# Performance work log

Measured on AMD Instinct MI355X. Metric: run time of the kernel, lower is better.

The kernel has to match this reference:

```python
import jax, jax.numpy as jnp
import numpy as np
import math

B, L, D = 8, 2048, 768
ORDER, EMB = 128, 5
FFT = 2 * L
MIN_DECAY = math.log(0.01) / 1.5   # slow_decay_pct = 1.5
MAX_DECAY = math.log(0.01) / 0.3   # fast_decay_pct = 0.3
SHIFT = 0.0


def _pos_emb(seq_len, emb_dim):
    # pos_emb_init from the source: [t, Re(z), Im(z)] with bands = (emb_dim-1)//2
    bands = (emb_dim - 1) // 2
    t = jnp.linspace(0.0, 1.0, seq_len)[None, :, None]
    t_res = jnp.linspace(0.0, seq_len - 1, seq_len)[None, :, None]
    w = 2.0 * jnp.pi * t_res / seq_len
    f = jnp.linspace(1e-4, bands - 1, bands)[None, None]
    zc = jnp.exp(-1j * f * w)
    return jnp.concatenate([t, zc.real, zc.imag], axis=-1).astype(jnp.float32)  # (1, L, EMB)


def setup_inputs() -> dict:
    key = jax.random.key(0)
    ks = jax.random.split(key, 16)
    s = 0.02
    return {
        "u": jax.random.normal(ks[0], (B, L, D), jnp.float32),
        "in_W": jax.random.normal(ks[1], (D, 3 * D), jnp.float32) * s,
        "in_b": jnp.zeros((3 * D,), jnp.float32),
        "out_W": jax.random.normal(ks[2], (D, D), jnp.float32) * s,
        "out_b": jnp.zeros((D,), jnp.float32),
        "x1_s": jax.random.normal(ks[3], (D, 4), jnp.float32) * 0.25,
        "x2_s": jax.random.normal(ks[4], (D, 4), jnp.float32) * 0.25,
        "v_s": jax.random.normal(ks[5], (D, 4), jnp.float32) * 0.25,
        "x1_sb": jax.random.normal(ks[6], (D,), jnp.float32) * 0.1,
        "x2_sb": jax.random.normal(ks[7], (D,), jnp.float32) * 0.1,
        "v_sb": jax.random.normal(ks[8], (D,), jnp.float32) * 0.1,
        "D_bias": jax.random.normal(ks[9], (D,), jnp.float32),
        "z": _pos_emb(L, EMB),
        "sin_freq": 10.0 * jnp.ones((1, ORDER), jnp.float32),   # hyena_w = 10
        "eo_mat": jax.random.normal(ks[10], (1, EMB, ORDER), jnp.float32) * 0.3,
        "eo_bias": jnp.zeros((1, ORDER), jnp.float32),
        "oo1_mat": jax.random.normal(ks[11], (1, ORDER, ORDER), jnp.float32) * 0.08,
        "oo1_bias": jnp.zeros((1, ORDER), jnp.float32),
        "oo2_mat": jax.random.normal(ks[12], (1, ORDER, ORDER), jnp.float32) * 0.08,
        "oo2_bias": jnp.zeros((1, ORDER), jnp.float32),
        "oh_mat": jax.random.normal(ks[13], (1, ORDER, D), jnp.float32) * 0.08,
    }


def _depthwise4(x, w, b):
    # torch Conv1d(groups=3D, kernel=4, padding=3) truncated to [:L] == causal conv, left pad 3
    out = jax.lax.conv_general_dilated(
        x, w[:, None, :], window_strides=(1,), padding=[(3, 0)],
        dimension_numbers=("NCH", "OIH", "NCH"), feature_group_count=x.shape[1])
    return out + b[None, :, None]


def _hyena_filter(z, sin_freq, eo_mat, eo_bias, oo1_mat, oo1_bias, oo2_mat, oo2_bias, oh_mat):
    # then exponential decay modulation (exp_mod_in_place_fwd), channels=1, reverse=0.
    f = sin_freq[:, None, :]                                       # (1, 1, ORDER)
    h = jnp.sin(f * (jnp.einsum("cle,ceo->clo", z, eo_mat) + eo_bias[:, None, :]))
    h = jnp.sin(f * (jnp.einsum("clo,cop->clp", h, oo1_mat) + oo1_bias[:, None, :]))
    h = jnp.sin(f * (jnp.einsum("clo,cop->clp", h, oo2_mat) + oo2_bias[:, None, :]))
    k = jnp.einsum("clo,coh->clh", h, oh_mat)                      # (1, L, D)
    t = jnp.linspace(0.0, 1.0, k.shape[1])
    deltas = jnp.abs(jnp.linspace(MIN_DECAY, MAX_DECAY, k.shape[2]))
    k = k * (jnp.exp(-t[None, :, None] * deltas[None, None, :]) + SHIFT)
    return k[0].T                                                  # (D, L)


def _forward(u, in_W, in_b, out_W, out_b, x1_s, x2_s, v_s, x1_sb, x2_sb, v_sb,
             D_bias, z, sin_freq, eo_mat, eo_bias, oo1_mat, oo1_bias,
             oo2_mat, oo2_bias, oh_mat):
    seqlen = u.shape[1]
    k = _hyena_filter(z, sin_freq, eo_mat, eo_bias, oo1_mat, oo1_bias, oo2_mat, oo2_bias, oh_mat)
    x1x2v = u @ in_W + in_b                                        # (B, L, 3D)
    x1, x2, v = jnp.split(x1x2v, 3, axis=-1)
    x1 = jnp.transpose(x1, (0, 2, 1))                              # (B, D, L)
    x2 = jnp.transpose(x2, (0, 2, 1))
    v = jnp.transpose(v, (0, 2, 1))
    x1 = _depthwise4(x1, x1_s, x1_sb)
    x2 = _depthwise4(x2, x2_s, x2_sb)
    v = _depthwise4(v, v_s, v_sb)
    v = v * x1                                                     # first gate
    k_f = jnp.fft.rfft(k.astype(jnp.float32), n=FFT)               # (D, FFT//2+1)
    v_f = jnp.fft.rfft(v.astype(jnp.float32), n=FFT)               # (B, D, FFT//2+1)
    y = jnp.fft.irfft(v_f * k_f[None], n=FFT)[..., :seqlen]        # long FFT conv
    y = y + v * D_bias[None, :, None]                              # skip term
    y = y * x2                                                     # second gate
    y = jnp.transpose(y, (0, 2, 1))                                # (B, L, D)
    return y @ out_W + out_b


def reference(u, in_W, in_b, out_W, out_b, x1_s, x2_s, v_s, x1_sb, x2_sb, v_sb,
              D_bias, z, sin_freq, eo_mat, eo_bias, oo1_mat, oo1_bias,
              oo2_mat, oo2_bias, oh_mat):
    return _forward(u, in_W, in_b, out_W, out_b, x1_s, x2_s, v_s, x1_sb, x2_sb, v_sb,
                    D_bias, z, sin_freq, eo_mat, eo_bias, oo1_mat, oo1_bias,
                    oo2_mat, oo2_bias, oh_mat)
```

## Files before the change

kernel.cpp:

```cpp
#include <hip/hip_runtime.h>


typedef __bf16 bf16x8 __attribute__((ext_vector_type(8)));
typedef float  f32x4  __attribute__((ext_vector_type(4)));

#define AS1 __attribute__((address_space(1)))
#define AS3 __attribute__((address_space(3)))
#define GLD16(gp, lp) __builtin_amdgcn_global_load_lds((AS1 void*)(void*)(gp), (AS3 void*)(void*)(lp), 16, 0, 0)

#define LGKM_BAR       __asm__ __volatile__("s_waitcnt lgkmcnt(0)\n\ts_barrier" ::: "memory")
#define VM_LGKM_BAR(N) __asm__ __volatile__("s_waitcnt vmcnt(" #N ") lgkmcnt(0)\n\ts_barrier" ::: "memory")

__device__ __forceinline__ unsigned short f2b(float f) {
    unsigned u = __builtin_bit_cast(unsigned, f);
    unsigned r = (u + 0x7fffu + ((u >> 16) & 1u)) >> 16;
    return (unsigned short)r;
}
__device__ __forceinline__ float b2f_lo(unsigned u) {
    return __builtin_bit_cast(float, u << 16);
}
__device__ __forceinline__ float b2f_hi(unsigned u) {
    return __builtin_bit_cast(float, u & 0xffff0000u);
}

__device__ __forceinline__ float2 cmul(float2 a, float2 b) {
    return make_float2(a.x * b.x - a.y * b.y, a.x * b.y + a.y * b.x);
}
__device__ __forceinline__ float2 cadd(float2 a, float2 b) { return make_float2(a.x + b.x, a.y + b.y); }
__device__ __forceinline__ float2 csub(float2 a, float2 b) { return make_float2(a.x - b.x, a.y - b.y); }

#define TWO_PI 6.283185307179586f

#define BFLY(i,j)   { float2 ta=x[i], tb=x[j]; x[i]=cadd(ta,tb); x[j]=csub(ta,tb); }
#define BFLYW(i,j,w){ float2 ta=x[i], tb=x[j]; x[i]=cadd(ta,tb); x[j]=cmul(csub(ta,tb),(w)); }
#define BFLYI(i,j)  { float2 ta=x[i], tb=x[j]; x[i]=cadd(ta,tb); float2 tt=csub(ta,tb); x[j]=make_float2(-dd*tt.y, dd*tt.x); }
#define CSWAP(i,j)  { float2 tt=x[i]; x[i]=x[j]; x[j]=tt; }

template<int DIR, bool UZ>
__device__ __forceinline__ void dft16(float2* x) {
    const float dd = (float)DIR;
    const float C1 = 0.92387953251128674f, S1 = 0.38268343236508977f, R2 = 0.70710678118654752f;
    const float2 W1 = make_float2( C1, dd*S1);
    const float2 W2 = make_float2( R2, dd*R2);
    const float2 W3 = make_float2( S1, dd*C1);
    const float2 W5 = make_float2(-S1, dd*C1);
    const float2 W6 = make_float2(-R2, dd*R2);
    const float2 W7 = make_float2(-C1, dd*S1);
    if (UZ) {
        x[8]  = x[0];
        x[9]  = cmul(x[1], W1);
        x[10] = cmul(x[2], W2);
        x[11] = cmul(x[3], W3);
        x[12] = make_float2(-dd*x[4].y, dd*x[4].x);
        x[13] = cmul(x[5], W5);
        x[14] = cmul(x[6], W6);
        x[15] = cmul(x[7], W7);
    } else {
        BFLY(0,8); BFLYW(1,9,W1); BFLYW(2,10,W2); BFLYW(3,11,W3);
        BFLYI(4,12); BFLYW(5,13,W5); BFLYW(6,14,W6); BFLYW(7,15,W7);
    }
    BFLY(0,4);  BFLYW(1,5,W2);  BFLYI(2,6);   BFLYW(3,7,W6);
    BFLY(8,12); BFLYW(9,13,W2); BFLYI(10,14); BFLYW(11,15,W6);
    BFLY(0,2);  BFLYI(1,3);  BFLY(4,6);   BFLYI(5,7);
    BFLY(8,10); BFLYI(9,11); BFLY(12,14); BFLYI(13,15);
    BFLY(0,1); BFLY(2,3); BFLY(4,5); BFLY(6,7);
    BFLY(8,9); BFLY(10,11); BFLY(12,13); BFLY(14,15);
    CSWAP(1,8); CSWAP(2,4); CSWAP(3,12); CSWAP(5,10); CSWAP(7,14); CSWAP(11,13);
}

__device__ __forceinline__ void twiddle16(float2* x, float ang) {
    float s, c; __sincosf(ang, &s, &c);
    const float2 u1  = make_float2(c, s);
    const float2 u2  = cmul(u1, u1);
    const float2 u3  = cmul(u2, u1);
    const float2 u4  = cmul(u2, u2);
    const float2 u8  = cmul(u4, u4);
    const float2 u12 = cmul(u8, u4);
    x[1]  = cmul(x[1],  u1);
    x[2]  = cmul(x[2],  u2);
    x[3]  = cmul(x[3],  u3);
    x[4]  = cmul(x[4],  u4);
    x[5]  = cmul(x[5],  cmul(u4, u1));
    x[6]  = cmul(x[6],  cmul(u4, u2));
    x[7]  = cmul(x[7],  cmul(u4, u3));
    x[8]  = cmul(x[8],  u8);
    x[9]  = cmul(x[9],  cmul(u8, u1));
    x[10] = cmul(x[10], cmul(u8, u2));
    x[11] = cmul(x[11], cmul(u8, u3));
    x[12] = cmul(x[12], u12);
    x[13] = cmul(x[13], cmul(u12, u1));
    x[14] = cmul(x[14], cmul(u12, u2));
    x[15] = cmul(x[15], cmul(u12, u3));
}

__device__ __forceinline__ int ph1(int row, int col) { return row * 256 + (col ^ row); }
__device__ __forceinline__ int ph2(int row, int col) { return row * 16 + (col ^ (row & 15)); }

__device__ __forceinline__ void fft4096_fwd(float2* x, float2* lds, int t) {
    dft16<-1, true>(x);
    twiddle16(x, -(float)t * (TWO_PI / 4096.0f));
    #pragma unroll
    for (int k1 = 0; k1 < 16; ++k1) lds[ph1(k1, t)] = x[k1];
    __syncthreads();
    const int hi = t >> 4, lo = t & 15;
    #pragma unroll
    for (int t1 = 0; t1 < 16; ++t1) x[t1] = lds[ph1(hi, t1 * 16 + lo)];
    dft16<-1, false>(x);
    twiddle16(x, -(float)lo * (TWO_PI / 256.0f));
    __syncthreads();
    #pragma unroll
    for (int k2 = 0; k2 < 16; ++k2) lds[ph2(t, k2)] = x[k2];
    __syncthreads();
    #pragma unroll
    for (int t0 = 0; t0 < 16; ++t0) x[t0] = lds[ph2(hi * 16 + t0, lo)];
    dft16<-1, false>(x);
}

__device__ __forceinline__ void fft4096_inv(float2* x, float2* lds, int t) {
    const int hi = t >> 4, lo = t & 15;
    dft16<1, false>(x);
    __syncthreads();
    #pragma unroll
    for (int t0 = 0; t0 < 16; ++t0) lds[ph2(hi * 16 + t0, lo)] = x[t0];
    __syncthreads();
    #pragma unroll
    for (int k2 = 0; k2 < 16; ++k2) x[k2] = lds[ph2(t, k2)];
    twiddle16(x, (float)lo * (TWO_PI / 256.0f));
    dft16<1, false>(x);
    __syncthreads();
    #pragma unroll
    for (int t1 = 0; t1 < 16; ++t1) lds[ph1(hi, t1 * 16 + lo)] = x[t1];
    __syncthreads();
    #pragma unroll
    for (int k1 = 0; k1 < 16; ++k1) x[k1] = lds[ph1(k1, t)];
    twiddle16(x, (float)t * (TWO_PI / 4096.0f));
    dft16<1, false>(x);
}

__global__ __launch_bounds__(256) void filter_k_kernel(
    const float* __restrict__ z, const float* __restrict__ sf,
    const float* __restrict__ eo, const float* __restrict__ eo_b,
    const float* __restrict__ oo1, const float* __restrict__ oo1_b,
    const float* __restrict__ oo2, const float* __restrict__ oo2_b,
    const float* __restrict__ oh, float* __restrict__ kfil)
{
    __shared__ float h3buf[4][128];
    __shared__ float htmp[2][128];
    const int t = threadIdx.x;
    const int l0 = blockIdx.x * 4;
    const int half = t >> 7;
    const int o = t & 127;
    const float sfo = sf[o];
    for (int p = 0; p < 2; ++p) {
        const int li = p * 2 + half;
        const int l = l0 + li;
        float a = eo_b[o];
        #pragma unroll
        for (int e = 0; e < 5; ++e) a += z[l * 5 + e] * eo[e * 128 + o];
        htmp[half][o] = sinf(sfo * a);
        __syncthreads();
        float a2 = oo1_b[o];
        for (int q = 0; q < 128; ++q) a2 += htmp[half][q] * oo1[q * 128 + o];
        const float h2 = sinf(sfo * a2);
        __syncthreads();
        htmp[half][o] = h2;
        __syncthreads();
        float a3 = oo2_b[o];
        for (int q = 0; q < 128; ++q) a3 += htmp[half][q] * oo2[q * 128 + o];
        h3buf[li][o] = sinf(sfo * a3);
        __syncthreads();
    }
    const float MIND = -3.070113457325394f;
    const float MAXD = -15.350567286626972f;
    for (int c = 0; c < 3; ++c) {
        const int h = t + c * 256;
        float acc[4];
        #pragma unroll
        for (int li = 0; li < 4; ++li) acc[li] = 0.f;
        for (int q = 0; q < 128; ++q) {
            const float w = oh[q * 768 + h];
            #pragma unroll
            for (int li = 0; li < 4; ++li) acc[li] += h3buf[li][q] * w;
        }
        const float delta = fabsf(MIND + (MAXD - MIND) * (float)h * (1.0f / 767.0f));
        #pragma unroll
        for (int li = 0; li < 4; ++li) {
            const int l = l0 + li;
            const float tt = (float)l * (1.0f / 2047.0f);
            kfil[h * 2048 + l] = acc[li] * expf(-tt * delta);
        }
    }
}

__global__ __launch_bounds__(256) void filter_fft_kernel(
    const float* __restrict__ kfil, const float* __restrict__ D_bias,
    float2* __restrict__ Kf)
{
    __shared__ __align__(16) float2 lds[4096];
    const int d = blockIdx.x, t = threadIdx.x;
    float2 x[16];
    #pragma unroll
    for (int r = 0; r < 8; ++r) x[r] = make_float2(kfil[d * 2048 + r * 256 + t], 0.f);
    fft4096_fwd(x, lds, t);
    const float db = D_bias[d];
    const float s = 1.0f / 4096.0f;
    #pragma unroll
    for (int k3 = 0; k3 < 16; ++k3)
        Kf[d * 4096 + k3 * 256 + t] = make_float2((x[k3].x + db) * s, x[k3].y * s);
}

__global__ __launch_bounds__(256) void convert_u_kernel(
    const float* __restrict__ u, unsigned short* __restrict__ ub)
{
    const int g = blockIdx.x * 256 + threadIdx.x;
    const float4 v = ((const float4*)u)[g];
    uint2 o;
    o.x = (unsigned)f2b(v.x) | ((unsigned)f2b(v.y) << 16);
    o.y = (unsigned)f2b(v.z) | ((unsigned)f2b(v.w) << 16);
    ((uint2*)ub)[g] = o;
}

__global__ __launch_bounds__(256) void transpose_W_kernel(
    const float* __restrict__ W, unsigned short* __restrict__ Wt, int K, int N)
{
    __shared__ float tile[32][33];
    const int n0 = blockIdx.x * 32, k0 = blockIdx.y * 32;
    const int tx = threadIdx.x & 31, ty = threadIdx.x >> 5;
    #pragma unroll
    for (int r = 0; r < 4; ++r) {
        const int kk = ty + r * 8;
        tile[kk][tx] = W[(k0 + kk) * N + n0 + tx];
    }
    __syncthreads();
    #pragma unroll
    for (int r = 0; r < 4; ++r) {
        const int nn = ty + r * 8;
        Wt[(n0 + nn) * K + k0 + tx] = f2b(tile[tx][nn]);
    }
}

__global__ __launch_bounds__(256) void transpose_Y_kernel(
    const unsigned short* __restrict__ Y, unsigned short* __restrict__ Yt)
{
    __shared__ unsigned short tile[32][34];
    const int bx = blockIdx.x;
    const int l0 = (bx & 63) * 32;
    const int tmp = bx >> 6;
    const int d0 = (tmp % 24) * 32;
    const int b  = tmp / 24;
    const int tx = threadIdx.x & 31, ty = threadIdx.x >> 5;
    #pragma unroll
    for (int r = 0; r < 4; ++r) {
        const int dd = ty + r * 8;
        tile[dd][tx] = Y[(b * 768 + d0 + dd) * 2048 + l0 + tx];
    }
    __syncthreads();
    #pragma unroll
    for (int r = 0; r < 4; ++r) {
        const int ll = ty + r * 8;
        Yt[(b * 2048 + l0 + ll) * 768 + d0 + tx] = tile[tx][ll];
    }
}

template<int TM, int TN, int WR, int WC, int MODE>
__global__ __launch_bounds__(512, 2) void gemm2ph_kernel(
    const unsigned short* __restrict__ A,
    const unsigned short* __restrict__ Bm,
    const float* __restrict__ bias,
    unsigned short* __restrict__ outb,
    float* __restrict__ outf)
{
    constexpr int MF = TM / WR / 16;
    constexpr int NF = TN / WC / 16;
    constexpr int QA = TM / 64;
    constexpr int QB = TN / 64;
    extern __shared__ __align__(16) unsigned short lds[];
    unsigned short* As = lds;
    unsigned short* Bs = lds + 2 * TM * 64;
    const int t = threadIdx.x;
    const int wv = t >> 6, lane = t & 63;
    const int row0 = (MODE == 0 ? blockIdx.y : blockIdx.x) * TM;
    const int col0 = (MODE == 0 ? blockIdx.x : blockIdx.y) * TN;
    const int wr = wv / WC, wc = wv % WC;
    const int frow = lane & 15, kc = lane >> 4;

    f32x4 acc[MF][NF] = {};

    const int srow = t >> 3;
    const int cdat = (t & 7) ^ (srow & 7);
    const unsigned short* gA = A  + (row0 + srow) * 768 + cdat * 8;
    const unsigned short* gB = Bm + (col0 + srow) * 768 + cdat * 8;

#define STAGE(buf, kt)                                                        \
    {                                                                         \
        _Pragma("unroll") for (int q = 0; q < QA; ++q)                        \
            GLD16(gA + q * 49152 + (kt) * 64,                                 \
                  (char*)As + (buf) * (TM * 128) + q * 8192 + wv * 1024);     \
        _Pragma("unroll") for (int q = 0; q < QB; ++q)                        \
            GLD16(gB + q * 49152 + (kt) * 64,                                 \
                  (char*)Bs + (buf) * (TN * 128) + q * 8192 + wv * 1024);     \
    }

#define HALF(buf, ks)                                                         \
    {                                                                         \
        bf16x8 aF[MF], bF[NF];                                                \
        _Pragma("unroll") for (int m = 0; m < MF; ++m) {                      \
            const int r = wr * (TM / WR) + m * 16 + frow;                     \
            aF[m] = *(const bf16x8*)(As + (buf) * (TM * 64) + r * 64 +        \
                                     ((((ks) * 4 + kc) ^ (r & 7)) << 3));     \
        }                                                                     \
        _Pragma("unroll") for (int n = 0; n < NF; ++n) {                      \
            const int r = wc * (TN / WC) + n * 16 + frow;                     \
            bF[n] = *(const bf16x8*)(Bs + (buf) * (TN * 64) + r * 64 +        \
                                     ((((ks) * 4 + kc) ^ (r & 7)) << 3));     \
        }                                                                     \
        __builtin_amdgcn_s_setprio(1);                                        \
        _Pragma("unroll") for (int m = 0; m < MF; ++m)                        \
        _Pragma("unroll") for (int n = 0; n < NF; ++n)                        \
            acc[m][n] = __builtin_amdgcn_mfma_f32_16x16x32_bf16(              \
                aF[m], bF[n], acc[m][n], 0, 0, 0);                            \
        __builtin_amdgcn_s_setprio(0);                                        \
    }

    STAGE(0, 0);
    STAGE(1, 1);
    VM_LGKM_BAR(7);

    HALF(0, 0); HALF(0, 1);
    VM_LGKM_BAR(0);

    #pragma unroll 1
    for (int kt = 1; kt <= 9; kt += 2) {
        STAGE(0, kt + 1);
        HALF(1, 0); HALF(1, 1);
        VM_LGKM_BAR(0);
        STAGE(1, kt + 2);
        HALF(0, 0); HALF(0, 1);
        VM_LGKM_BAR(0);
    }

    HALF(1, 0); HALF(1, 1);
#undef STAGE
#undef HALF

    if (MODE == 0) {
        const int part = row0 / 768;
        const int bb = col0 / 2048;
        unsigned short* Xp = outb + (size_t)(part * 8 + bb) * 768 * 2048;
        const int drow0 = row0 - part * 768 + wr * (TM / WR) + kc * 4;
        const int lcol0 = col0 - bb * 2048 + wc * (TN / WC) + frow;
        #pragma unroll
        for (int m = 0; m < MF; ++m) {
            #pragma unroll
            for (int rr = 0; rr < 4; ++rr) {
                const int dd = drow0 + m * 16 + rr;
                const float bn = bias[row0 + wr * (TM / WR) + kc * 4 + m * 16 + rr];
                #pragma unroll
                for (int n = 0; n < NF; ++n)
                    Xp[dd * 2048 + lcol0 + n * 16] = f2b(acc[m][n][rr] + bn);
            }
        }
    } else {
        #pragma unroll
        for (int m = 0; m < MF; ++m) {
            #pragma unroll
            for (int rr = 0; rr < 4; ++rr) {
                const int mm = row0 + wr * (TM / WR) + kc * 4 + m * 16 + rr;
                #pragma unroll
                for (int n = 0; n < NF; ++n) {
                    const int nn = col0 + wc * (TN / WC) + n * 16 + frow;
                    outf[(size_t)mm * 768 + nn] = acc[m][n][rr] + bias[nn];
                }
            }
        }
    }
}

__device__ __forceinline__ void conv6(const unsigned short* __restrict__ p,
                                      const float* w, float bias, int t, float* out8)
{
    const uint4 m = *(const uint4*)(p + 8 * t);
    uint2 q = make_uint2(0u, 0u);
    if (t) q = *(const uint2*)(p + 8 * t - 4);
    float s[12];
    s[0] = b2f_lo(q.x); s[1] = b2f_hi(q.x); s[2] = b2f_lo(q.y); s[3] = b2f_hi(q.y);
    s[4] = b2f_lo(m.x); s[5] = b2f_hi(m.x); s[6] = b2f_lo(m.y); s[7] = b2f_hi(m.y);
    s[8] = b2f_lo(m.z); s[9] = b2f_hi(m.z); s[10] = b2f_lo(m.w); s[11] = b2f_hi(m.w);
    #pragma unroll
    for (int i = 0; i < 8; ++i)
        out8[i] = bias + w[0] * s[i + 1] + w[1] * s[i + 2] + w[2] * s[i + 3] + w[3] * s[i + 4];
}

__global__ __launch_bounds__(256) void fft_conv_kernel(
    const unsigned short* __restrict__ X, const float2* __restrict__ Kf,
    const float* __restrict__ x1_s, const float* __restrict__ x2_s, const float* __restrict__ v_s,
    const float* __restrict__ x1_sb, const float* __restrict__ x2_sb, const float* __restrict__ v_sb,
    unsigned short* __restrict__ Y)
{
    __shared__ __align__(16) float2 lds[4096];
    unsigned* ldsu = (unsigned*)lds;
    const int d = blockIdx.x, jp = blockIdx.y, t = threadIdx.x;
    const int b0 = jp * 2, b1 = b0 + 1;

    const unsigned short* px1a = X + ((size_t)(0 * 8 + b0) * 768 + d) * 2048;
    const unsigned short* pva  = X + ((size_t)(2 * 8 + b0) * 768 + d) * 2048;
    const unsigned short* px1b = X + ((size_t)(0 * 8 + b1) * 768 + d) * 2048;
    const unsigned short* pvb  = X + ((size_t)(2 * 8 + b1) * 768 + d) * 2048;

    {
        float w1[4], wv[4];
        #pragma unroll
        for (int j = 0; j < 4; ++j) { w1[j] = x1_s[d * 4 + j]; wv[j] = v_s[d * 4 + j]; }
        const float bc1 = x1_sb[d], bcv = v_sb[d];
        float pa[8];
        {
            float va[8], g[8];
            conv6(pva,  wv, bcv, t, va);
            conv6(px1a, w1, bc1, t, g);
            #pragma unroll
            for (int i = 0; i < 8; ++i) pa[i] = va[i] * g[i];
        }
        {
            float vb[8], g[8];
            conv6(pvb,  wv, bcv, t, vb);
            conv6(px1b, w1, bc1, t, g);
            unsigned vh[8];
            #pragma unroll
            for (int i = 0; i < 8; ++i)
                vh[i] = (unsigned)f2b(pa[i]) | ((unsigned)f2b(vb[i] * g[i]) << 16);
            *(uint4*)(ldsu + 8 * t)     = make_uint4(vh[0], vh[1], vh[2], vh[3]);
            *(uint4*)(ldsu + 8 * t + 4) = make_uint4(vh[4], vh[5], vh[6], vh[7]);
        }
    }
    __syncthreads();

    float2 x[16];
    #pragma unroll
    for (int r = 0; r < 8; ++r) {
        const unsigned u = ldsu[r * 256 + t];
        x[r] = make_float2(b2f_lo(u), b2f_hi(u));
    }
    __syncthreads();

    fft4096_fwd(x, lds, t);

    {
        const float2* kf = Kf + (size_t)d * 4096;
        #pragma unroll
        for (int c4 = 0; c4 < 4; ++c4) {
            float2 kr[4];
            #pragma unroll
            for (int j = 0; j < 4; ++j) kr[j] = kf[(c4 * 4 + j) * 256 + t];
            #pragma unroll
            for (int j = 0; j < 4; ++j) x[c4 * 4 + j] = cmul(x[c4 * 4 + j], kr[j]);
            __asm__ __volatile__("" ::: "memory");
        }
    }

    fft4096_inv(x, lds, t);

    __syncthreads();
    {
        const unsigned short* px2a = X + ((size_t)(1 * 8 + b0) * 768 + d) * 2048;
        const unsigned short* px2b = X + ((size_t)(1 * 8 + b1) * 768 + d) * 2048;
        float w2[4];
        #pragma unroll
        for (int j = 0; j < 4; ++j) w2[j] = x2_s[d * 4 + j];
        const float bc2 = x2_sb[d];
        float ga[8], gb[8];
        conv6(px2a, w2, bc2, t, ga);
        conv6(px2b, w2, bc2, t, gb);
        unsigned c2[8];
        #pragma unroll
        for (int i = 0; i < 8; ++i)
            c2[i] = (unsigned)f2b(ga[i]) | ((unsigned)f2b(gb[i]) << 16);
        *(uint4*)(ldsu + 8 * t)     = make_uint4(c2[0], c2[1], c2[2], c2[3]);
        *(uint4*)(ldsu + 8 * t + 4) = make_uint4(c2[4], c2[5], c2[6], c2[7]);
    }
    __syncthreads();

    unsigned short* ya = Y + ((size_t)b0 * 768 + d) * 2048;
    unsigned short* yb = Y + ((size_t)b1 * 768 + d) * 2048;
    #pragma unroll
    for (int n1 = 0; n1 < 8; ++n1) {
        const int l = n1 * 256 + t;
        const unsigned u = ldsu[l];
        ya[l] = f2b(x[n1].x * b2f_lo(u));
        yb[l] = f2b(x[n1].y * b2f_hi(u));
    }
}

extern "C" void kernel_launch(void* const* d_in, const int* in_sizes, int n_in,
                              void* d_out, int out_size, void* d_ws, size_t ws_size,
                              hipStream_t stream)
{
    (void)in_sizes; (void)n_in; (void)out_size; (void)ws_size;
    const float* u      = (const float*)d_in[0];
    const float* in_W   = (const float*)d_in[1];
    const float* in_b   = (const float*)d_in[2];
    const float* out_W  = (const float*)d_in[3];
    const float* out_b  = (const float*)d_in[4];
    const float* x1_s   = (const float*)d_in[5];
    const float* x2_s   = (const float*)d_in[6];
    const float* v_s    = (const float*)d_in[7];
    const float* x1_sb  = (const float*)d_in[8];
    const float* x2_sb  = (const float*)d_in[9];
    const float* v_sb   = (const float*)d_in[10];
    const float* D_bias = (const float*)d_in[11];
    const float* z      = (const float*)d_in[12];
    const float* sf     = (const float*)d_in[13];
    const float* eo     = (const float*)d_in[14];
    const float* eo_b   = (const float*)d_in[15];
    const float* oo1    = (const float*)d_in[16];
    const float* oo1_b  = (const float*)d_in[17];
    const float* oo2    = (const float*)d_in[18];
    const float* oo2_b  = (const float*)d_in[19];
    const float* oh     = (const float*)d_in[20];
    float* out = (float*)d_out;

    char* ws = (char*)d_ws;
    unsigned short* Xbf  = (unsigned short*)(ws + 0);
    unsigned short* Ybf  = (unsigned short*)(ws + 75497472);
    unsigned short* ubYt = (unsigned short*)(ws + 100663296);
    unsigned short* Wt   = (unsigned short*)(ws + 125829120);
    unsigned short* W2t  = (unsigned short*)(ws + 129368064);
    float*          kfil = (float*)(ws + 130547712);
    float2*         Kf   = (float2*)(ws + 136839168);

    static int attr_set = 0;
    if (!attr_set) {
        (void)hipFuncSetAttribute(
            reinterpret_cast<const void*>(&gemm2ph_kernel<192, 256, 2, 4, 0>),
            hipFuncAttributeMaxDynamicSharedMemorySize, 114688);
        (void)hipFuncSetAttribute(
            reinterpret_cast<const void*>(&gemm2ph_kernel<256, 192, 4, 2, 1>),
            hipFuncAttributeMaxDynamicSharedMemorySize, 114688);
        attr_set = 1;
    }

    filter_k_kernel<<<512, 256, 0, stream>>>(z, sf, eo, eo_b, oo1, oo1_b, oo2, oo2_b, oh, kfil);
    filter_fft_kernel<<<768, 256, 0, stream>>>(kfil, D_bias, Kf);
    convert_u_kernel<<<12288, 256, 0, stream>>>(u, ubYt);
    transpose_W_kernel<<<dim3(72, 24), 256, 0, stream>>>(in_W, Wt, 768, 2304);
    transpose_W_kernel<<<dim3(24, 24), 256, 0, stream>>>(out_W, W2t, 768, 768);
    gemm2ph_kernel<192, 256, 2, 4, 0><<<dim3(64, 12), 512, 114688, stream>>>(
        Wt, ubYt, in_b, Xbf, nullptr);
    fft_conv_kernel<<<dim3(768, 4), 256, 0, stream>>>(Xbf, Kf, x1_s, x2_s, v_s, x1_sb, x2_sb, v_sb, Ybf);
    transpose_Y_kernel<<<12288, 256, 0, stream>>>(Ybf, ubYt);
    gemm2ph_kernel<256, 192, 4, 2, 1><<<dim3(64, 4), 512, 114688, stream>>>(
        ubYt, W2t, out_b, nullptr, out);
}
```

Before: 348.2 us.

## Restructure GEMM main loop into eight-phase interleaved load/MFMA schedule

Replaces the two-phase double-buffered GEMM loop with an eight-phase schedule. Each K tile is split into four quadrant MFMA groups, and the A and B global-to-LDS loads are spread between them with finer barriers. The aim is to overlap global loads, LDS reads and MFMA work more evenly, so matrix cores are not stalled at the coarse barriers. In exchange it adds more barriers, more complex waitcnt accounting and a higher risk of ordering bugs in the buffer reuse.

```diff
diff --git a/kernel.cpp b/kernel.cpp
--- a/kernel.cpp
+++ b/kernel.cpp
@@ -263,7 +263,7 @@
 }
 
 template<int TM, int TN, int WR, int WC, int MODE>
-__global__ __launch_bounds__(512, 2) void gemm2ph_kernel(
+__global__ __launch_bounds__(512, 2) void gemm8ph_kernel(
     const unsigned short* __restrict__ A,
     const unsigned short* __restrict__ Bm,
     const float* __restrict__ bias,
@@ -272,6 +272,8 @@
 {
     constexpr int MF = TM / WR / 16;
     constexpr int NF = TN / WC / 16;
+    constexpr int MH = MF / 2;
+    constexpr int NH = NF / 2;
     constexpr int QA = TM / 64;
     constexpr int QB = TN / 64;
     extern __shared__ __align__(16) unsigned short lds[];
@@ -291,57 +293,115 @@
     const unsigned short* gA = A  + (row0 + srow) * 768 + cdat * 8;
     const unsigned short* gB = Bm + (col0 + srow) * 768 + cdat * 8;
 
-#define STAGE(buf, kt)                                                        \
-    {                                                                         \
-        _Pragma("unroll") for (int q = 0; q < QA; ++q)                        \
-            GLD16(gA + q * 49152 + (kt) * 64,                                 \
-                  (char*)As + (buf) * (TM * 128) + q * 8192 + wv * 1024);     \
-        _Pragma("unroll") for (int q = 0; q < QB; ++q)                        \
-            GLD16(gB + q * 49152 + (kt) * 64,                                 \
-                  (char*)Bs + (buf) * (TN * 128) + q * 8192 + wv * 1024);     \
-    }
-
-#define HALF(buf, ks)                                                         \
-    {                                                                         \
-        bf16x8 aF[MF], bF[NF];                                                \
-        _Pragma("unroll") for (int m = 0; m < MF; ++m) {                      \
-            const int r = wr * (TM / WR) + m * 16 + frow;                     \
-            aF[m] = *(const bf16x8*)(As + (buf) * (TM * 64) + r * 64 +        \
-                                     ((((ks) * 4 + kc) ^ (r & 7)) << 3));     \
-        }                                                                     \
-        _Pragma("unroll") for (int n = 0; n < NF; ++n) {                      \
-            const int r = wc * (TN / WC) + n * 16 + frow;                     \
-            bF[n] = *(const bf16x8*)(Bs + (buf) * (TN * 64) + r * 64 +        \
-                                     ((((ks) * 4 + kc) ^ (r & 7)) << 3));     \
-        }                                                                     \
-        __builtin_amdgcn_s_setprio(1);                                        \
-        _Pragma("unroll") for (int m = 0; m < MF; ++m)                        \
-        _Pragma("unroll") for (int n = 0; n < NF; ++n)                        \
-            acc[m][n] = __builtin_amdgcn_mfma_f32_16x16x32_bf16(              \
-                aF[m], bF[n], acc[m][n], 0, 0, 0);                            \
-        __builtin_amdgcn_s_setprio(0);                                        \
-    }
-
-    STAGE(0, 0);
-    STAGE(1, 1);
-    VM_LGKM_BAR(7);
-
-    HALF(0, 0); HALF(0, 1);
-    VM_LGKM_BAR(0);
+#define STG_Aq(buf, q, kt) GLD16(gA + (q) * 49152 + (kt),                     \
+        (char*)As + (buf) * (TM * 128) + (q) * 8192 + wv * 1024)
+#define STG_Bq(buf, q, kt) GLD16(gB + (q) * 49152 + (kt),                     \
+        (char*)Bs + (buf) * (TN * 128) + (q) * 8192 + wv * 1024)
+#define STG_A1(buf, kt) { STG_Aq(buf, 0, kt); STG_Aq(buf, 1, kt); }
+#define STG_A2(buf, kt) { _Pragma("unroll") for (int q = 2; q < QA; ++q) STG_Aq(buf, q, kt); }
+#define STG_B1(buf, kt) { STG_Bq(buf, 0, kt); STG_Bq(buf, 1, kt); }
+#define STG_B2(buf, kt) { _Pragma("unroll") for (int q = 2; q < QB; ++q) STG_Bq(buf, q, kt); }
+#define FENCE_QB { if constexpr (QB == 4) { VM_LGKM_BAR(4); } else { VM_LGKM_BAR(3); } }
+
+    bf16x8 aF[MH][2], bN0[NH][2], bN1[NH][2];
+
+#define READ_A(buf, mh)                                                        \
+    _Pragma("unroll") for (int m = 0; m < MH; ++m) {                           \
+        const int r = wr * (TM / WR) + ((mh) * MH + m) * 16 + frow;            \
+        aF[m][0] = *(const bf16x8*)(As + (buf) * (TM * 64) + r * 64 +          \
+                                    (((0 + kc) ^ (r & 7)) << 3));              \
+        aF[m][1] = *(const bf16x8*)(As + (buf) * (TM * 64) + r * 64 +          \
+                                    (((4 + kc) ^ (r & 7)) << 3));              \
+    }
+#define READ_B(buf, nh, arr)                                                   \
+    _Pragma("unroll") for (int n = 0; n < NH; ++n) {                           \
+        const int r = wc * (TN / WC) + ((nh) * NH + n) * 16 + frow;            \
+        arr[n][0] = *(const bf16x8*)(Bs + (buf) * (TN * 64) + r * 64 +         \
+                                     (((0 + kc) ^ (r & 7)) << 3));             \
+        arr[n][1] = *(const bf16x8*)(Bs + (buf) * (TN * 64) + r * 64 +         \
+                                     (((4 + kc) ^ (r & 7)) << 3));             \
+    }
+#define MFMA_Q(mh, nh, arr)                                                    \
+    __builtin_amdgcn_s_setprio(1);                                             \
+    _Pragma("unroll") for (int m = 0; m < MH; ++m)                             \
+    _Pragma("unroll") for (int n = 0; n < NH; ++n)                             \
+    _Pragma("unroll") for (int ks = 0; ks < 2; ++ks)                           \
+        acc[(mh) * MH + m][(nh) * NH + n] =                                    \
+            __builtin_amdgcn_mfma_f32_16x16x32_bf16(                           \
+                aF[m][ks], arr[n][ks], acc[(mh) * MH + m][(nh) * NH + n],      \
+                0, 0, 0);                                                      \
+    __builtin_amdgcn_s_setprio(0);
+
+    STG_A1(0, 0); STG_A2(0, 0); STG_B1(0, 0); STG_B2(0, 0);
+    STG_B1(1, 64); STG_B2(1, 64);
+    FENCE_QB;
 
     #pragma unroll 1
-    for (int kt = 1; kt <= 9; kt += 2) {
-        STAGE(0, kt + 1);
-        HALF(1, 0); HALF(1, 1);
+    for (int i = 0; i < 5; ++i) {
+        const int k1 = (2 * i + 1) * 64, k2 = (2 * i + 2) * 64, k3 = (2 * i + 3) * 64;
+        READ_A(0, 0); READ_B(0, 0, bN0);
+        STG_A1(1, k1);
+        MFMA_Q(0, 0, bN0);
+        LGKM_BAR;
+        READ_B(0, 1, bN1);
+        STG_A2(1, k1);
+        MFMA_Q(0, 1, bN1);
+        LGKM_BAR;
+        READ_A(0, 1);
+        STG_B1(0, k2);
+        MFMA_Q(1, 1, bN1);
+        LGKM_BAR;
+        STG_B2(0, k2);
+        MFMA_Q(1, 0, bN0);
+        FENCE_QB;
+        READ_A(1, 0); READ_B(1, 0, bN0);
+        STG_A1(0, k2);
+        MFMA_Q(0, 0, bN0);
+        LGKM_BAR;
+        READ_B(1, 1, bN1);
+        STG_A2(0, k2);
+        MFMA_Q(0, 1, bN1);
+        LGKM_BAR;
+        READ_A(1, 1);
+        STG_B1(1, k3);
+        MFMA_Q(1, 1, bN1);
+        LGKM_BAR;
+        STG_B2(1, k3);
+        MFMA_Q(1, 0, bN0);
+        FENCE_QB;
+    }
+
+    {
+        READ_A(0, 0); READ_B(0, 0, bN0);
+        STG_A1(1, 704);
+        MFMA_Q(0, 0, bN0);
+        LGKM_BAR;
+        READ_B(0, 1, bN1);
+        STG_A2(1, 704);
+        MFMA_Q(0, 1, bN1);
+        LGKM_BAR;
+        READ_A(0, 1);
+        MFMA_Q(1, 1, bN1);
+        LGKM_BAR;
+        MFMA_Q(1, 0, bN0);
         VM_LGKM_BAR(0);
-        STAGE(1, kt + 2);
-        HALF(0, 0); HALF(0, 1);
-        VM_LGKM_BAR(0);
-    }
-
-    HALF(1, 0); HALF(1, 1);
-#undef STAGE
-#undef HALF
+        READ_A(1, 0); READ_B(1, 0, bN0); READ_B(1, 1, bN1);
+        MFMA_Q(0, 0, bN0);
+        MFMA_Q(0, 1, bN1);
+        READ_A(1, 1);
+        MFMA_Q(1, 1, bN1);
+        MFMA_Q(1, 0, bN0);
+    }
+#undef READ_A
+#undef READ_B
+#undef MFMA_Q
+#undef STG_Aq
+#undef STG_Bq
+#undef STG_A1
+#undef STG_A2
+#undef STG_B1
+#undef STG_B2
+#undef FENCE_QB
 
     if (MODE == 0) {
         const int part = row0 / 768;
@@ -530,10 +590,10 @@
     static int attr_set = 0;
     if (!attr_set) {
         (void)hipFuncSetAttribute(
-            reinterpret_cast<const void*>(&gemm2ph_kernel<192, 256, 2, 4, 0>),
+            reinterpret_cast<const void*>(&gemm8ph_kernel<192, 256, 2, 4, 0>),
             hipFuncAttributeMaxDynamicSharedMemorySize, 114688);
         (void)hipFuncSetAttribute(
-            reinterpret_cast<const void*>(&gemm2ph_kernel<256, 192, 4, 2, 1>),
+            reinterpret_cast<const void*>(&gemm8ph_kernel<256, 192, 4, 2, 1>),
             hipFuncAttributeMaxDynamicSharedMemorySize, 114688);
         attr_set = 1;
     }
@@ -543,10 +603,10 @@
     convert_u_kernel<<<12288, 256, 0, stream>>>(u, ubYt);
     transpose_W_kernel<<<dim3(72, 24), 256, 0, stream>>>(in_W, Wt, 768, 2304);
     transpose_W_kernel<<<dim3(24, 24), 256, 0, stream>>>(out_W, W2t, 768, 768);
-    gemm2ph_kernel<192, 256, 2, 4, 0><<<dim3(64, 12), 512, 114688, stream>>>(
+    gemm8ph_kernel<192, 256, 2, 4, 0><<<dim3(64, 12), 512, 114688, stream>>>(
         Wt, ubYt, in_b, Xbf, nullptr);
     fft_conv_kernel<<<dim3(768, 4), 256, 0, stream>>>(Xbf, Kf, x1_s, x2_s, v_s, x1_sb, x2_sb, v_sb, Ybf);
     transpose_Y_kernel<<<12288, 256, 0, stream>>>(Ybf, ubYt);
-    gemm2ph_kernel<256, 192, 4, 2, 1><<<dim3(64, 4), 512, 114688, stream>>>(
+    gemm8ph_kernel<256, 192, 4, 2, 1><<<dim3(64, 4), 512, 114688, stream>>>(
         ubYt, W2t, out_b, nullptr, out);
 }
```

Result: slower. 361.3 us (+3.8%).

## Load in-projection GEMM B operand directly into registers, bypassing LDS

Applied to the files above, without the earlier changes.

Replaces the MODE-0 in-projection GEMM with a dedicated kernel that stages only the weight (A) tile through LDS. The B operand (the u activations) is loaded from global memory straight into MFMA register fragments, double-buffered across k-steps. This cuts LDS capacity per block (49 KB instead of 112 KB) and removes the LDS round trip for B. In exchange it adds register pressure and makes more direct, less coalesced global loads, with waitcnt values tuned by hand.

```diff
diff --git a/kernel.cpp b/kernel.cpp
--- a/kernel.cpp
+++ b/kernel.cpp
@@ -262,12 +262,122 @@
     }
 }
 
-template<int TM, int TN, int WR, int WC, int MODE>
+__global__ __launch_bounds__(512, 2) void gemm_bd_kernel(
+    const unsigned short* __restrict__ A,
+    const unsigned short* __restrict__ Bm,
+    const float* __restrict__ bias,
+    unsigned short* __restrict__ outb)
+{
+    extern __shared__ __align__(16) unsigned short lds[];
+    unsigned short* As = lds;
+    const int t = threadIdx.x;
+    const int wv = t >> 6, lane = t & 63;
+    const int row0 = blockIdx.y * 192;
+    const int col0 = blockIdx.x * 256;
+    const int wr = wv >> 2, wc = wv & 3;
+    const int frow = lane & 15, kc = lane >> 4;
+
+    f32x4 acc[6][4] = {};
+
+    const int srow = t >> 3;
+    const int cdat = (t & 7) ^ (srow & 7);
+    const unsigned short* gA = A + (row0 + srow) * 768 + cdat * 8;
+
+#define STG_A(buf, kt)                                                        \
+    { _Pragma("unroll") for (int q = 0; q < 3; ++q)                           \
+        GLD16(gA + q * 49152 + (kt) * 64,                                     \
+              (char*)As + (buf) * 24576 + q * 8192 + wv * 1024); }
+
+    const unsigned short* pB = Bm + (size_t)(col0 + wc * 64 + frow) * 768 + kc * 8;
+    bf16x8 bR0[4][2], bR1[4][2];
+
+#define LOADB(BR, tt)                                                         \
+    { _Pragma("unroll") for (int n = 0; n < 4; ++n) {                         \
+        BR[n][0] = *(const bf16x8*)(pB + (size_t)n * 12288 + (tt) * 64);      \
+        BR[n][1] = *(const bf16x8*)(pB + (size_t)n * 12288 + (tt) * 64 + 32); \
+    } }
+
+#define COMPUTE_HALF(bufbit, BR, mh)                                          \
+    {                                                                         \
+        bf16x8 aF[3][2];                                                      \
+        _Pragma("unroll") for (int m = 0; m < 3; ++m) {                       \
+            const int r = wr * 96 + ((mh) * 3 + m) * 16 + frow;               \
+            aF[m][0] = *(const bf16x8*)(As + (bufbit) * 12288 + r * 64 +      \
+                                        (((0 + kc) ^ (r & 7)) << 3));         \
+            aF[m][1] = *(const bf16x8*)(As + (bufbit) * 12288 + r * 64 +      \
+                                        (((4 + kc) ^ (r & 7)) << 3));         \
+        }                                                                     \
+        __builtin_amdgcn_s_setprio(1);                                        \
+        _Pragma("unroll") for (int m = 0; m < 3; ++m)                         \
+        _Pragma("unroll") for (int n = 0; n < 4; ++n)                         \
+        _Pragma("unroll") for (int ks = 0; ks < 2; ++ks)                      \
+            acc[(mh) * 3 + m][n] = __builtin_amdgcn_mfma_f32_16x16x32_bf16(   \
+                aF[m][ks], BR[n][ks], acc[(mh) * 3 + m][n], 0, 0, 0);         \
+        __builtin_amdgcn_s_setprio(0);                                        \
+    }
+
+    STG_A(0, 0);
+    LOADB(bR0, 0);
+    STG_A(1, 1);
+    LOADB(bR1, 1);
+    VM_LGKM_BAR(11);
+
+    COMPUTE_HALF(0, bR0, 0); COMPUTE_HALF(0, bR0, 1);
+    LOADB(bR0, 2);
+    VM_LGKM_BAR(8);
+
+    #pragma unroll 1
+    for (int i = 0; i < 4; ++i) {
+        const int to = 2 * i + 1, te = 2 * i + 2;
+        STG_A(0, to + 1);
+        COMPUTE_HALF(1, bR1, 0); COMPUTE_HALF(1, bR1, 1);
+        LOADB(bR1, to + 2);
+        VM_LGKM_BAR(8);
+        STG_A(1, te + 1);
+        COMPUTE_HALF(0, bR0, 0); COMPUTE_HALF(0, bR0, 1);
+        LOADB(bR0, te + 2);
+        VM_LGKM_BAR(8);
+    }
+
+    STG_A(0, 10);
+    COMPUTE_HALF(1, bR1, 0); COMPUTE_HALF(1, bR1, 1);
+    LOADB(bR1, 11);
+    VM_LGKM_BAR(8);
+
+    STG_A(1, 11);
+    COMPUTE_HALF(0, bR0, 0); COMPUTE_HALF(0, bR0, 1);
+    VM_LGKM_BAR(0);
+
+    COMPUTE_HALF(1, bR1, 0); COMPUTE_HALF(1, bR1, 1);
+#undef STG_A
+#undef LOADB
+#undef COMPUTE_HALF
+
+    {
+        const int part = row0 / 768;
+        const int bb = col0 / 2048;
+        unsigned short* Xp = outb + (size_t)(part * 8 + bb) * 768 * 2048;
+        const int drow0 = row0 - part * 768 + wr * 96 + kc * 4;
+        const int lcol0 = col0 - bb * 2048 + wc * 64 + frow;
+        #pragma unroll
+        for (int m = 0; m < 6; ++m) {
+            #pragma unroll
+            for (int rr = 0; rr < 4; ++rr) {
+                const int dd = drow0 + m * 16 + rr;
+                const float bn = bias[row0 + wr * 96 + kc * 4 + m * 16 + rr];
+                #pragma unroll
+                for (int n = 0; n < 4; ++n)
+                    Xp[dd * 2048 + lcol0 + n * 16] = f2b(acc[m][n][rr] + bn);
+            }
+        }
+    }
+}
+
+template<int TM, int TN, int WR, int WC>
 __global__ __launch_bounds__(512, 2) void gemm2ph_kernel(
     const unsigned short* __restrict__ A,
     const unsigned short* __restrict__ Bm,
     const float* __restrict__ bias,
-    unsigned short* __restrict__ outb,
     float* __restrict__ outf)
 {
     constexpr int MF = TM / WR / 16;
@@ -279,8 +389,8 @@
     unsigned short* Bs = lds + 2 * TM * 64;
     const int t = threadIdx.x;
     const int wv = t >> 6, lane = t & 63;
-    const int row0 = (MODE == 0 ? blockIdx.y : blockIdx.x) * TM;
-    const int col0 = (MODE == 0 ? blockIdx.x : blockIdx.y) * TN;
+    const int row0 = blockIdx.x * TM;
+    const int col0 = blockIdx.y * TN;
     const int wr = wv / WC, wc = wv % WC;
     const int frow = lane & 15, kc = lane >> 4;
 
@@ -343,34 +453,15 @@
 #undef STAGE
 #undef HALF
 
-    if (MODE == 0) {
-        const int part = row0 / 768;
-        const int bb = col0 / 2048;
-        unsigned short* Xp = outb + (size_t)(part * 8 + bb) * 768 * 2048;
-        const int drow0 = row0 - part * 768 + wr * (TM / WR) + kc * 4;
-        const int lcol0 = col0 - bb * 2048 + wc * (TN / WC) + frow;
-        #pragma unroll
-        for (int m = 0; m < MF; ++m) {
+    #pragma unroll
+    for (int m = 0; m < MF; ++m) {
+        #pragma unroll
+        for (int rr = 0; rr < 4; ++rr) {
+            const int mm = row0 + wr * (TM / WR) + kc * 4 + m * 16 + rr;
             #pragma unroll
-            for (int rr = 0; rr < 4; ++rr) {
-                const int dd = drow0 + m * 16 + rr;
-                const float bn = bias[row0 + wr * (TM / WR) + kc * 4 + m * 16 + rr];
-                #pragma unroll
-                for (int n = 0; n < NF; ++n)
-                    Xp[dd * 2048 + lcol0 + n * 16] = f2b(acc[m][n][rr] + bn);
-            }
-        }
-    } else {
-        #pragma unroll
-        for (int m = 0; m < MF; ++m) {
-            #pragma unroll
-            for (int rr = 0; rr < 4; ++rr) {
-                const int mm = row0 + wr * (TM / WR) + kc * 4 + m * 16 + rr;
-                #pragma unroll
-                for (int n = 0; n < NF; ++n) {
-                    const int nn = col0 + wc * (TN / WC) + n * 16 + frow;
-                    outf[(size_t)mm * 768 + nn] = acc[m][n][rr] + bias[nn];
-                }
+            for (int n = 0; n < NF; ++n) {
+                const int nn = col0 + wc * (TN / WC) + n * 16 + frow;
+                outf[(size_t)mm * 768 + nn] = acc[m][n][rr] + bias[nn];
             }
         }
     }
@@ -530,10 +621,10 @@
     static int attr_set = 0;
     if (!attr_set) {
         (void)hipFuncSetAttribute(
-            reinterpret_cast<const void*>(&gemm2ph_kernel<192, 256, 2, 4, 0>),
-            hipFuncAttributeMaxDynamicSharedMemorySize, 114688);
+            reinterpret_cast<const void*>(&gemm_bd_kernel),
+            hipFuncAttributeMaxDynamicSharedMemorySize, 49152);
         (void)hipFuncSetAttribute(
-            reinterpret_cast<const void*>(&gemm2ph_kernel<256, 192, 4, 2, 1>),
+            reinterpret_cast<const void*>(&gemm2ph_kernel<256, 192, 4, 2>),
             hipFuncAttributeMaxDynamicSharedMemorySize, 114688);
         attr_set = 1;
     }
@@ -543,10 +634,9 @@
     convert_u_kernel<<<12288, 256, 0, stream>>>(u, ubYt);
     transpose_W_kernel<<<dim3(72, 24), 256, 0, stream>>>(in_W, Wt, 768, 2304);
     transpose_W_kernel<<<dim3(24, 24), 256, 0, stream>>>(out_W, W2t, 768, 768);
-    gemm2ph_kernel<192, 256, 2, 4, 0><<<dim3(64, 12), 512, 114688, stream>>>(
-        Wt, ubYt, in_b, Xbf, nullptr);
+    gemm_bd_kernel<<<dim3(64, 12), 512, 49152, stream>>>(Wt, ubYt, in_b, Xbf);
     fft_conv_kernel<<<dim3(768, 4), 256, 0, stream>>>(Xbf, Kf, x1_s, x2_s, v_s, x1_sb, x2_sb, v_sb, Ybf);
     transpose_Y_kernel<<<12288, 256, 0, stream>>>(Ybf, ubYt);
-    gemm2ph_kernel<256, 192, 4, 2, 1><<<dim3(64, 4), 512, 114688, stream>>>(
-        ubYt, W2t, out_b, nullptr, out);
-}
+    gemm2ph_kernel<256, 192, 4, 2><<<dim3(64, 4), 512, 114688, stream>>>(
+        ubYt, W2t, out_b, out);
+}
```

New measurement: 390.1 us. 1.12x slower.
